# Optimization experiments

Measured on AMD Instinct MI355X. Metric: run time of the kernel, lower is better.

## Reference

```python
import jax, jax.numpy as jnp
import numpy as np
from jax import lax

R = 512          # num RoIs
K = 81           # num classes (COCO + bg)
IM_H, IM_W = 800, 1333
WX, WY, WW, WH = 10.0, 10.0, 5.0, 5.0   # cfg.MODEL.BBOX_REG_WEIGHTS
XFORM_CLIP = float(np.log(1000.0 / 16.0))  # cfg.BBOX_XFORM_CLIP
NMS_THRESH = 0.5
SCORE_THRESH = 0.001
MAX_PER_IMG = 100
POST_NMS_TOPN = 300


def setup_inputs() -> dict:
    key = jax.random.key(0)
    k1, k2, k3, k4, k5, k6 = jax.random.split(key, 6)
    # Build valid RoIs inside the image (x1<x2, y1<y2)
    cx = jax.random.uniform(k1, (R,)) * IM_W
    cy = jax.random.uniform(k2, (R,)) * IM_H
    w = jax.random.uniform(k3, (R,)) * 200.0 + 20.0
    h = jax.random.uniform(k4, (R,)) * 200.0 + 20.0
    rois = jnp.stack([
        jnp.clip(cx - 0.5 * w, 0.0, IM_W - 1),
        jnp.clip(cy - 0.5 * h, 0.0, IM_H - 1),
        jnp.clip(cx + 0.5 * w, 0.0, IM_W - 1),
        jnp.clip(cy + 0.5 * h, 0.0, IM_H - 1),
    ], axis=1).astype(jnp.float32)
    deltas = (jax.random.normal(k5, (R, 4 * K)) * 0.3).astype(jnp.float32)
    scores = jax.nn.softmax(jax.random.normal(k6, (R, K)) * 2.0, axis=1).astype(jnp.float32)
    return {"rois": rois, "deltas": deltas, "scores": scores}


def bbox_transform(boxes, deltas):
    # boxes [R,4], deltas [R,4K] -> pred boxes [R,K,4], clamped to image
    widths = boxes[:, 2] - boxes[:, 0] + 1.0
    heights = boxes[:, 3] - boxes[:, 1] + 1.0
    ctr_x = boxes[:, 0] + 0.5 * widths
    ctr_y = boxes[:, 1] + 0.5 * heights
    d = deltas.reshape(-1, K, 4)  # [R,K,4]
    dx = d[:, :, 0] / WX
    dy = d[:, :, 1] / WY
    dw = jnp.minimum(d[:, :, 2] / WW, XFORM_CLIP)
    dh = jnp.minimum(d[:, :, 3] / WH, XFORM_CLIP)
    pcx = dx * widths[:, None] + ctr_x[:, None]
    pcy = dy * heights[:, None] + ctr_y[:, None]
    pw = jnp.exp(dw) * widths[:, None]
    ph = jnp.exp(dh) * heights[:, None]
    x1 = jnp.clip(pcx - 0.5 * pw, 0.0, IM_W - 1)
    y1 = jnp.clip(pcy - 0.5 * ph, 0.0, IM_H - 1)
    x2 = jnp.clip(pcx + 0.5 * pw - 1.0, 0.0, IM_W - 1)
    y2 = jnp.clip(pcy + 0.5 * ph - 1.0, 0.0, IM_H - 1)
    return jnp.stack([x1, y1, x2, y2], axis=-1)  # [R,K,4]


def nms_one_class(scores_c, boxes_c):
    # Greedy NMS for one class. scores_c [R], boxes_c [R,4] -> keep mask [R] (orig order)
    order = jnp.argsort(-scores_c)
    b = boxes_c[order]
    areas = (b[:, 2] - b[:, 0] + 1.0) * (b[:, 3] - b[:, 1] + 1.0)
    xx1 = jnp.maximum(b[:, None, 0], b[None, :, 0])
    yy1 = jnp.maximum(b[:, None, 1], b[None, :, 1])
    xx2 = jnp.minimum(b[:, None, 2], b[None, :, 2])
    yy2 = jnp.minimum(b[:, None, 3], b[None, :, 3])
    inter = jnp.maximum(xx2 - xx1 + 1.0, 0.0) * jnp.maximum(yy2 - yy1 + 1.0, 0.0)
    iou = inter / (areas[:, None] + areas[None, :] - inter)
    suppress = iou > NMS_THRESH  # [R,R]
    idx = jnp.arange(R)

    def body(i, keep):
        sup = suppress[i] & keep[i] & (idx > i)
        return keep & (~sup)

    keep = lax.fori_loop(0, R, body, jnp.ones((R,), bool))
    keep = keep & (jnp.cumsum(keep) <= POST_NMS_TOPN)
    return jnp.zeros((R,), bool).at[order].set(keep)


def _detect(rois, deltas, scores):
    boxes3 = bbox_transform(rois, deltas)  # [R,K,4]
    # valid classes: max score over rois (excluding bg) above threshold
    cls_valid = jnp.concatenate([
        jnp.zeros((1,), bool),
        scores[:, 1:].max(axis=0) > SCORE_THRESH,
    ])  # [K]
    keep_kc = jax.vmap(nms_one_class, in_axes=(1, 1))(scores, boxes3)  # [K,R]
    nms_mask = (keep_kc.T & cls_valid[None, :]).astype(scores.dtype)  # [R,K]
    dists_all = nms_mask * scores
    # duplicate filtering: one label per box
    scores_pre = dists_all.max(axis=1)   # [R]
    labels_pre = dists_all.argmax(axis=1)
    order = jnp.argsort(-scores_pre)
    top = order[:MAX_PER_IMG]            # [100]
    scores_all = scores_pre[top]
    labels_all = labels_pre[top]
    valid = scores_all > SCORE_THRESH
    boxes_assign = boxes3.reshape(-1, 4)[top * K + labels_all]  # [100,4]
    scores_all = jnp.where(valid, scores_all, 0.0)
    boxes_assign = jnp.where(valid[:, None], boxes_assign, 0.0)
    out = jnp.concatenate([scores_all[:, None], boxes_assign], axis=1)  # [100,5]
    return out, labels_all, top


def reference(rois, deltas, scores):
    return _detect(rois, deltas, scores)
```

## Files before the change

### kernel.cpp

```cpp
#include <hip/hip_runtime.h>
#include <cstdint>
#include <cstddef>


#define R 512
#define K 81
#define IM_W_MAX 1332.0f
#define IM_H_MAX 799.0f
#define XFORM_CLIP_F 4.135166556742356f
#define NMS_THRESH_F 0.5f
#define SCORE_THRESH_F 0.001f
#define MAX_PER_IMG 100
#define POST_NMS_TOPN 300

__device__ __forceinline__ float4 transform_box(const float* __restrict__ rois,
                                                const float* __restrict__ deltas,
                                                int r, int k) {
    float4 roi = ((const float4*)rois)[r];
    float4 d4  = *(const float4*)(deltas + (size_t)r * (4 * K) + 4 * k);
    float w  = roi.z - roi.x + 1.0f;
    float h  = roi.w - roi.y + 1.0f;
    float cx = roi.x + 0.5f * w;
    float cy = roi.y + 0.5f * h;
    float dx = d4.x / 10.0f;
    float dy = d4.y / 10.0f;
    float dw = fminf(d4.z / 5.0f, XFORM_CLIP_F);
    float dh = fminf(d4.w / 5.0f, XFORM_CLIP_F);
    float pcx = dx * w + cx;
    float pcy = dy * h + cy;
    float pw  = expf(dw) * w;
    float ph  = expf(dh) * h;
    float4 b;
    b.x = fminf(fmaxf(pcx - 0.5f * pw, 0.0f), IM_W_MAX);
    b.y = fminf(fmaxf(pcy - 0.5f * ph, 0.0f), IM_H_MAX);
    b.z = fminf(fmaxf(pcx + 0.5f * pw - 1.0f, 0.0f), IM_W_MAX);
    b.w = fminf(fmaxf(pcy + 0.5f * ph - 1.0f, 0.0f), IM_H_MAX);
    return b;
}

__global__ void __launch_bounds__(512)
rank_boxes_kernel(const float* __restrict__ rois,
                  const float* __restrict__ deltas,
                  const float* __restrict__ scores,
                  float4* __restrict__ sbox_g,
                  int* __restrict__ order_g,
                  float* __restrict__ ssc_g,
                  int* __restrict__ valid_g) {
    const int k = blockIdx.x, tid = threadIdx.x;
    __shared__ unsigned long long s_key[R];
    __shared__ float s_red[R];

    const float sc = scores[tid * K + k];
    {
        unsigned int bits = __float_as_uint(sc);
        s_key[tid] = ((unsigned long long)(~bits) << 32) | (unsigned int)tid;
    }
    s_red[tid] = sc;
    __syncthreads();
    for (int s = 256; s > 0; s >>= 1) {
        if (tid < s) s_red[tid] = fmaxf(s_red[tid], s_red[tid + s]);
        __syncthreads();
    }
    const bool valid = (k != 0) && (s_red[0] > SCORE_THRESH_F);
    if (tid == 0) valid_g[k] = valid;
    if (!valid) return;

    const unsigned long long ki = s_key[tid];
    int cnt = 0;
    const ulonglong2* kp = (const ulonglong2*)s_key;
    #pragma unroll 8
    for (int j2 = 0; j2 < R / 2; ++j2) {
        ulonglong2 k2 = kp[j2];
        cnt += (k2.x < ki);
        cnt += (k2.y < ki);
    }
    sbox_g[k * R + cnt]  = transform_box(rois, deltas, tid, k);
    order_g[k * R + cnt] = tid;
    ssc_g[k * R + cnt]   = sc;
}

__device__ __forceinline__ bool iou_sup(float4 bi, float ai, float4 bj, float aj) {
    float xx1 = fmaxf(bi.x, bj.x);
    float yy1 = fmaxf(bi.y, bj.y);
    float xx2 = fminf(bi.z, bj.z);
    float yy2 = fminf(bi.w, bj.w);
    float iw = fmaxf(xx2 - xx1 + 1.0f, 0.0f);
    float ih = fmaxf(yy2 - yy1 + 1.0f, 0.0f);
    float inter = iw * ih;
    float denom = ai + aj - inter;
    float two_i = inter + inter;
    bool sup = two_i > denom * 1.0000002f;
    if (!sup && !(two_i < denom * 0.99999976f)) {
        sup = (inter / denom) > NMS_THRESH_F;
    }
    return sup;
}

__global__ void __launch_bounds__(256)
bitmatrix_kernel(const float4* __restrict__ sbox_g,
                 const int* __restrict__ valid_g,
                 unsigned long long* __restrict__ supT_g) {
    const int b = blockIdx.x;
    const int k = b >> 3;
    const int w = b & 7;
    const int tid = threadIdx.x;
    if (!valid_g[k]) return;

    __shared__ float4 s_jbox[64];
    __shared__ float  s_jarea[64];

    const int jbase = w * 64;
    if (tid < 64) {
        float4 bx = sbox_g[k * R + jbase + tid];
        s_jbox[tid]  = bx;
        s_jarea[tid] = (bx.z - bx.x + 1.0f) * (bx.w - bx.y + 1.0f);
    }

    const int i0 = tid;
    const float4 bi0 = sbox_g[k * R + i0];
    const float  ai0 = (bi0.z - bi0.x + 1.0f) * (bi0.w - bi0.y + 1.0f);

    const unsigned long long* dummy;
    (void)dummy;

    if (w < 4) {
        __syncthreads();
        const int d0 = i0 - jbase;
        unsigned long long mask0 =
            (d0 < 0) ? ~0ull : ((d0 >= 63) ? 0ull : (~0ull << (d0 + 1)));
        unsigned long long bits0 = 0ull;
        if (mask0) {
            #pragma unroll 8
            for (int jj = 0; jj < 64; ++jj) {
                float4 bj = s_jbox[jj];
                float  aj = s_jarea[jj];
                bits0 |= (unsigned long long)iou_sup(bi0, ai0, bj, aj) << jj;
            }
        }
        supT_g[k * 4096 + w * 512 + i0]       = bits0 & mask0;
        supT_g[k * 4096 + w * 512 + i0 + 256] = 0ull;
    } else {
        const int i1 = i0 + 256;
        const float4 bi1 = sbox_g[k * R + i1];
        const float  ai1 = (bi1.z - bi1.x + 1.0f) * (bi1.w - bi1.y + 1.0f);
        __syncthreads();
        const int d1 = i1 - jbase;
        unsigned long long mask1 =
            (d1 < 0) ? ~0ull : ((d1 >= 63) ? 0ull : (~0ull << (d1 + 1)));
        unsigned long long bits0 = 0ull, bits1 = 0ull;
        if (__ballot(mask1 != 0ull)) {
            #pragma unroll 8
            for (int jj = 0; jj < 64; ++jj) {
                float4 bj = s_jbox[jj];
                float  aj = s_jarea[jj];
                bits0 |= (unsigned long long)iou_sup(bi0, ai0, bj, aj) << jj;
                bits1 |= (unsigned long long)iou_sup(bi1, ai1, bj, aj) << jj;
            }
        } else {
            #pragma unroll 8
            for (int jj = 0; jj < 64; ++jj) {
                float4 bj = s_jbox[jj];
                float  aj = s_jarea[jj];
                bits0 |= (unsigned long long)iou_sup(bi0, ai0, bj, aj) << jj;
            }
        }
        supT_g[k * 4096 + w * 512 + i0] = bits0;
        supT_g[k * 4096 + w * 512 + i1] = bits1 & mask1;
    }
}

__global__ void __launch_bounds__(64)
sweep_kernel(const unsigned long long* __restrict__ supT_g,
             const int* __restrict__ order_g,
             const float* __restrict__ ssc_g,
             const int* __restrict__ valid_g,
             float* __restrict__ dists_t) {
    const int k = blockIdx.x;
    const int l = threadIdx.x;

    if (!valid_g[k]) {
        #pragma unroll
        for (int p = 0; p < 8; ++p) dists_t[k * R + p * 64 + l] = 0.0f;
        return;
    }

    int   ord[8];
    float ssc[8];
    #pragma unroll
    for (int p = 0; p < 8; ++p) {
        ord[p] = order_g[k * R + p * 64 + l];
        ssc[p] = ssc_g[k * R + p * 64 + l];
    }

    const unsigned long long* base = supT_g + (size_t)k * 4096;
    unsigned long long rrow[8], rnext[8];
    #pragma unroll
    for (int w = 0; w < 8; ++w) rrow[w] = base[w * 512 + l];

    unsigned long long kb[8];
    #pragma unroll
    for (int w = 0; w < 8; ++w) kb[w] = ~0ull;

    #pragma unroll
    for (int wb = 0; wb < 8; ++wb) {
        if (wb < 7) {
            #pragma unroll
            for (int w = 0; w < 8; ++w)
                rnext[w] = (w > wb) ? base[w * 512 + (wb + 1) * 64 + l] : 0ull;
        }

        const unsigned long long nz = __ballot(rrow[wb] != 0ull);
        unsigned long long cur = kb[wb];
        unsigned long long m = cur & nz;
        while (m) {
            int bit = __builtin_ctzll(m);
            const unsigned int r_lo = (unsigned int)(rrow[wb] & 0xffffffffull);
            const unsigned int r_hi = (unsigned int)(rrow[wb] >> 32);
            unsigned long long row =
                ((unsigned long long)(unsigned int)__builtin_amdgcn_readlane((int)r_hi, bit) << 32) |
                 (unsigned long long)(unsigned int)__builtin_amdgcn_readlane((int)r_lo, bit);
            m &= m - 1;
            cur &= ~row;
            m   &= ~row;
        }
        kb[wb] = cur;

        #pragma unroll
        for (int w = wb + 1; w < 8; ++w) {
            unsigned long long contrib = ((cur >> l) & 1ull) ? rrow[w] : 0ull;
            if (__ballot(contrib != 0ull)) {
                #pragma unroll
                for (int off = 32; off > 0; off >>= 1)
                    contrib |= __shfl_xor(contrib, off, 64);
                kb[w] &= ~contrib;
            }
        }

        #pragma unroll
        for (int w = 0; w < 8; ++w) rrow[w] = rnext[w];
    }

    int total = 0;
    #pragma unroll
    for (int w = 0; w < 8; ++w) total += __popcll(kb[w]);
    if (total > POST_NMS_TOPN) {
        int cnt = 0;
        #pragma unroll
        for (int w = 0; w < 8; ++w) {
            int pc = __popcll(kb[w]);
            if (cnt + pc <= POST_NMS_TOPN) { cnt += pc; continue; }
            unsigned long long word = kb[w], outw = 0ull;
            int room = POST_NMS_TOPN - cnt;
            while (room > 0) {
                unsigned long long lsb = word & (~word + 1ull);
                outw |= lsb; word ^= lsb; --room;
            }
            kb[w] = outw; cnt = POST_NMS_TOPN;
        }
    }

    #pragma unroll
    for (int p = 0; p < 8; ++p)
        dists_t[k * R + ord[p]] = ((kb[p] >> l) & 1ull) ? ssc[p] : 0.0f;
}

__global__ void __launch_bounds__(512)
finalize_kernel(const float* __restrict__ dists_t,
                const float* __restrict__ rois,
                const float* __restrict__ deltas,
                float* __restrict__ out) {
    const int b = blockIdx.x;
    const int t = threadIdx.x;
    __shared__ unsigned long long s_key[R];
    __shared__ int s_arg[R];

    {
        const int r = t;
        float vmax = dists_t[r];
        int arg = 0;
        #pragma unroll 8
        for (int kk = 1; kk < K; ++kk) {
            float v = dists_t[kk * R + r];
            if (v > vmax) { vmax = v; arg = kk; }
        }
        unsigned int bits = __float_as_uint(vmax);
        s_key[r] = ((unsigned long long)(~bits) << 32) | (unsigned int)r;
        s_arg[r] = arg;
    }
    __syncthreads();

    const int ri = b * 64 + (t >> 3);
    const int c  = t & 7;
    const unsigned long long ki = s_key[ri];
    int cnt = 0;
    #pragma unroll 8
    for (int j = 0; j < 64; ++j) {
        int jj = (j + c * 8) & 63;
        cnt += (s_key[c * 64 + jj] < ki);
    }
    cnt += __shfl_xor(cnt, 1, 64);
    cnt += __shfl_xor(cnt, 2, 64);
    cnt += __shfl_xor(cnt, 4, 64);

    if (c == 0 && cnt < MAX_PER_IMG) {
        float vmax = __uint_as_float(~(unsigned int)(ki >> 32));
        int arg = s_arg[ri];
        bool valid = vmax > SCORE_THRESH_F;
        float4 bx = transform_box(rois, deltas, ri, arg);
        out[cnt * 5 + 0] = valid ? vmax : 0.0f;
        out[cnt * 5 + 1] = valid ? bx.x : 0.0f;
        out[cnt * 5 + 2] = valid ? bx.y : 0.0f;
        out[cnt * 5 + 3] = valid ? bx.z : 0.0f;
        out[cnt * 5 + 4] = valid ? bx.w : 0.0f;
        out[500 + cnt] = (float)arg;
        out[600 + cnt] = (float)ri;
    }
}

extern "C" void kernel_launch(void* const* d_in, const int* in_sizes, int n_in,
                              void* d_out, int out_size, void* d_ws, size_t ws_size,
                              hipStream_t stream) {
    const float* rois   = (const float*)d_in[0];
    const float* deltas = (const float*)d_in[1];
    const float* scores = (const float*)d_in[2];
    float* out = (float*)d_out;

    char* ws = (char*)d_ws;
    float4* sbox_g  = (float4*)(ws + 0);
    int*    order_g = (int*)   (ws + 663552);
    float*  ssc_g   = (float*) (ws + 829440);
    int*    valid_g = (int*)   (ws + 995328);
    float*  dists_t = (float*) (ws + 995840);
    unsigned long long* supT_g = (unsigned long long*)(ws + 1161728);

    rank_boxes_kernel<<<K, 512, 0, stream>>>(rois, deltas, scores,
                                             sbox_g, order_g, ssc_g, valid_g);
    bitmatrix_kernel <<<K * 8, 256, 0, stream>>>(sbox_g, valid_g, supT_g);
    sweep_kernel     <<<K, 64, 0, stream>>>(supT_g, order_g, ssc_g, valid_g, dists_t);
    finalize_kernel  <<<8, 512, 0, stream>>>(dists_t, rois, deltas, out);
}
```

Measured before the change: 106.0 us.

## Fuse NMS bitmatrix and sweep kernels with a last-block-done counter

Merges the suppression bitmatrix kernel and the greedy sweep kernel into one launch. Each class's 8 blocks bump a per-class atomic counter, and the last block to finish runs the sweep for that class, reading the bitmatrix with agent-scope atomic loads. This removes one kernel launch and its inter-kernel gap, and lets sweeps for early classes overlap with bitmatrix work for other classes. It also drops the redundant zero stores for the unused lower-triangle words. The cost is a per-class counter reset in the rank kernel. There is some memory-ordering risk, because the stores are relaxed and no explicit fence comes before the counter increment.

```diff
diff --git a/kernel.cpp b/kernel.cpp
--- a/kernel.cpp
+++ b/kernel.cpp
@@ -12,6 +12,15 @@
 #define SCORE_THRESH_F 0.001f
 #define MAX_PER_IMG 100
 #define POST_NMS_TOPN 300
+
+__device__ __forceinline__ void store_agent_u64(unsigned long long* p,
+                                                unsigned long long v) {
+    __hip_atomic_store(p, v, __ATOMIC_RELAXED, __HIP_MEMORY_SCOPE_AGENT);
+}
+__device__ __forceinline__ unsigned long long load_agent_u64(
+        const unsigned long long* p) {
+    return __hip_atomic_load(p, __ATOMIC_RELAXED, __HIP_MEMORY_SCOPE_AGENT);
+}
 
 __device__ __forceinline__ float4 transform_box(const float* __restrict__ rois,
                                                 const float* __restrict__ deltas,
@@ -38,47 +47,6 @@
     return b;
 }
 
-__global__ void __launch_bounds__(512)
-rank_boxes_kernel(const float* __restrict__ rois,
-                  const float* __restrict__ deltas,
-                  const float* __restrict__ scores,
-                  float4* __restrict__ sbox_g,
-                  int* __restrict__ order_g,
-                  float* __restrict__ ssc_g,
-                  int* __restrict__ valid_g) {
-    const int k = blockIdx.x, tid = threadIdx.x;
-    __shared__ unsigned long long s_key[R];
-    __shared__ float s_red[R];
-
-    const float sc = scores[tid * K + k];
-    {
-        unsigned int bits = __float_as_uint(sc);
-        s_key[tid] = ((unsigned long long)(~bits) << 32) | (unsigned int)tid;
-    }
-    s_red[tid] = sc;
-    __syncthreads();
-    for (int s = 256; s > 0; s >>= 1) {
-        if (tid < s) s_red[tid] = fmaxf(s_red[tid], s_red[tid + s]);
-        __syncthreads();
-    }
-    const bool valid = (k != 0) && (s_red[0] > SCORE_THRESH_F);
-    if (tid == 0) valid_g[k] = valid;
-    if (!valid) return;
-
-    const unsigned long long ki = s_key[tid];
-    int cnt = 0;
-    const ulonglong2* kp = (const ulonglong2*)s_key;
-    #pragma unroll 8
-    for (int j2 = 0; j2 < R / 2; ++j2) {
-        ulonglong2 k2 = kp[j2];
-        cnt += (k2.x < ki);
-        cnt += (k2.y < ki);
-    }
-    sbox_g[k * R + cnt]  = transform_box(rois, deltas, tid, k);
-    order_g[k * R + cnt] = tid;
-    ssc_g[k * R + cnt]   = sc;
-}
-
 __device__ __forceinline__ bool iou_sup(float4 bi, float ai, float4 bj, float aj) {
     float xx1 = fmaxf(bi.x, bj.x);
     float yy1 = fmaxf(bi.y, bj.y);
@@ -96,89 +64,134 @@
     return sup;
 }
 
+__global__ void __launch_bounds__(512)
+rank_boxes_kernel(const float* __restrict__ rois,
+                  const float* __restrict__ deltas,
+                  const float* __restrict__ scores,
+                  float4* __restrict__ sbox_g,
+                  int* __restrict__ order_g,
+                  float* __restrict__ ssc_g,
+                  int* __restrict__ valid_g,
+                  int* __restrict__ done_k) {
+    const int k = blockIdx.x, tid = threadIdx.x;
+    __shared__ unsigned long long s_key[R];
+    __shared__ float s_red[R];
+
+    const float sc = scores[tid * K + k];
+    {
+        unsigned int bits = __float_as_uint(sc);
+        s_key[tid] = ((unsigned long long)(~bits) << 32) | (unsigned int)tid;
+    }
+    s_red[tid] = sc;
+    __syncthreads();
+    for (int s = 256; s > 0; s >>= 1) {
+        if (tid < s) s_red[tid] = fmaxf(s_red[tid], s_red[tid + s]);
+        __syncthreads();
+    }
+    const bool valid = (k != 0) && (s_red[0] > SCORE_THRESH_F);
+    if (tid == 0) { valid_g[k] = valid; done_k[k] = 0; }
+    if (!valid) return;
+
+    const unsigned long long ki = s_key[tid];
+    int cnt = 0;
+    const ulonglong2* kp = (const ulonglong2*)s_key;
+    #pragma unroll 8
+    for (int j2 = 0; j2 < R / 2; ++j2) {
+        ulonglong2 k2 = kp[j2];
+        cnt += (k2.x < ki);
+        cnt += (k2.y < ki);
+    }
+    sbox_g[k * R + cnt]  = transform_box(rois, deltas, tid, k);
+    order_g[k * R + cnt] = tid;
+    ssc_g[k * R + cnt]   = sc;
+}
+
 __global__ void __launch_bounds__(256)
-bitmatrix_kernel(const float4* __restrict__ sbox_g,
-                 const int* __restrict__ valid_g,
-                 unsigned long long* __restrict__ supT_g) {
+bitmega_kernel(const float4* __restrict__ sbox_g,
+               const int* __restrict__ valid_g,
+               unsigned long long* __restrict__ supT_g,
+               const int* __restrict__ order_g,
+               const float* __restrict__ ssc_g,
+               int* __restrict__ done_k,
+               float* __restrict__ dists_t) {
     const int b = blockIdx.x;
     const int k = b >> 3;
     const int w = b & 7;
     const int tid = threadIdx.x;
-    if (!valid_g[k]) return;
 
     __shared__ float4 s_jbox[64];
     __shared__ float  s_jarea[64];
-
+    __shared__ int    s_closer;
+
+    const bool valid = valid_g[k] != 0;
     const int jbase = w * 64;
-    if (tid < 64) {
-        float4 bx = sbox_g[k * R + jbase + tid];
-        s_jbox[tid]  = bx;
-        s_jarea[tid] = (bx.z - bx.x + 1.0f) * (bx.w - bx.y + 1.0f);
-    }
-
-    const int i0 = tid;
-    const float4 bi0 = sbox_g[k * R + i0];
-    const float  ai0 = (bi0.z - bi0.x + 1.0f) * (bi0.w - bi0.y + 1.0f);
-
-    const unsigned long long* dummy;
-    (void)dummy;
-
-    if (w < 4) {
+
+    if (valid) {
+        if (tid < 64) {
+            float4 bx = sbox_g[k * R + jbase + tid];
+            s_jbox[tid]  = bx;
+            s_jarea[tid] = (bx.z - bx.x + 1.0f) * (bx.w - bx.y + 1.0f);
+        }
+        const int i0 = tid;
+        const float4 bi0 = sbox_g[k * R + i0];
+        const float  ai0 = (bi0.z - bi0.x + 1.0f) * (bi0.w - bi0.y + 1.0f);
+
+        if (w < 4) {
+            __syncthreads();
+            const int d0 = i0 - jbase;
+            unsigned long long mask0 =
+                (d0 < 0) ? ~0ull : ((d0 >= 63) ? 0ull : (~0ull << (d0 + 1)));
+            unsigned long long bits0 = 0ull;
+            if (mask0) {
+                #pragma unroll 8
+                for (int jj = 0; jj < 64; ++jj) {
+                    float4 bj = s_jbox[jj];
+                    float  aj = s_jarea[jj];
+                    bits0 |= (unsigned long long)iou_sup(bi0, ai0, bj, aj) << jj;
+                }
+            }
+            store_agent_u64(&supT_g[k * 4096 + w * 512 + i0], bits0 & mask0);
+        } else {
+            const int i1 = i0 + 256;
+            const float4 bi1 = sbox_g[k * R + i1];
+            const float  ai1 = (bi1.z - bi1.x + 1.0f) * (bi1.w - bi1.y + 1.0f);
+            __syncthreads();
+            const int d1 = i1 - jbase;
+            unsigned long long mask1 =
+                (d1 < 0) ? ~0ull : ((d1 >= 63) ? 0ull : (~0ull << (d1 + 1)));
+            unsigned long long bits0 = 0ull, bits1 = 0ull;
+            if (__ballot(mask1 != 0ull)) {
+                #pragma unroll 8
+                for (int jj = 0; jj < 64; ++jj) {
+                    float4 bj = s_jbox[jj];
+                    float  aj = s_jarea[jj];
+                    bits0 |= (unsigned long long)iou_sup(bi0, ai0, bj, aj) << jj;
+                    bits1 |= (unsigned long long)iou_sup(bi1, ai1, bj, aj) << jj;
+                }
+            } else {
+                #pragma unroll 8
+                for (int jj = 0; jj < 64; ++jj) {
+                    float4 bj = s_jbox[jj];
+                    float  aj = s_jarea[jj];
+                    bits0 |= (unsigned long long)iou_sup(bi0, ai0, bj, aj) << jj;
+                }
+            }
+            store_agent_u64(&supT_g[k * 4096 + w * 512 + i0], bits0);
+            store_agent_u64(&supT_g[k * 4096 + w * 512 + i1], bits1 & mask1);
+        }
+    } else {
         __syncthreads();
-        const int d0 = i0 - jbase;
-        unsigned long long mask0 =
-            (d0 < 0) ? ~0ull : ((d0 >= 63) ? 0ull : (~0ull << (d0 + 1)));
-        unsigned long long bits0 = 0ull;
-        if (mask0) {
-            #pragma unroll 8
-            for (int jj = 0; jj < 64; ++jj) {
-                float4 bj = s_jbox[jj];
-                float  aj = s_jarea[jj];
-                bits0 |= (unsigned long long)iou_sup(bi0, ai0, bj, aj) << jj;
-            }
-        }
-        supT_g[k * 4096 + w * 512 + i0]       = bits0 & mask0;
-        supT_g[k * 4096 + w * 512 + i0 + 256] = 0ull;
-    } else {
-        const int i1 = i0 + 256;
-        const float4 bi1 = sbox_g[k * R + i1];
-        const float  ai1 = (bi1.z - bi1.x + 1.0f) * (bi1.w - bi1.y + 1.0f);
-        __syncthreads();
-        const int d1 = i1 - jbase;
-        unsigned long long mask1 =
-            (d1 < 0) ? ~0ull : ((d1 >= 63) ? 0ull : (~0ull << (d1 + 1)));
-        unsigned long long bits0 = 0ull, bits1 = 0ull;
-        if (__ballot(mask1 != 0ull)) {
-            #pragma unroll 8
-            for (int jj = 0; jj < 64; ++jj) {
-                float4 bj = s_jbox[jj];
-                float  aj = s_jarea[jj];
-                bits0 |= (unsigned long long)iou_sup(bi0, ai0, bj, aj) << jj;
-                bits1 |= (unsigned long long)iou_sup(bi1, ai1, bj, aj) << jj;
-            }
-        } else {
-            #pragma unroll 8
-            for (int jj = 0; jj < 64; ++jj) {
-                float4 bj = s_jbox[jj];
-                float  aj = s_jarea[jj];
-                bits0 |= (unsigned long long)iou_sup(bi0, ai0, bj, aj) << jj;
-            }
-        }
-        supT_g[k * 4096 + w * 512 + i0] = bits0;
-        supT_g[k * 4096 + w * 512 + i1] = bits1 & mask1;
-    }
-}
-
-__global__ void __launch_bounds__(64)
-sweep_kernel(const unsigned long long* __restrict__ supT_g,
-             const int* __restrict__ order_g,
-             const float* __restrict__ ssc_g,
-             const int* __restrict__ valid_g,
-             float* __restrict__ dists_t) {
-    const int k = blockIdx.x;
-    const int l = threadIdx.x;
-
-    if (!valid_g[k]) {
+    }
+
+    __syncthreads();
+    if (tid == 0) s_closer = (atomicAdd(&done_k[k], 1) == 7);
+    __syncthreads();
+    if (!s_closer) return;
+
+    if (tid >= 64) return;
+    const int l = tid;
+
+    if (!valid) {
         #pragma unroll
         for (int p = 0; p < 8; ++p) dists_t[k * R + p * 64 + l] = 0.0f;
         return;
@@ -192,21 +205,23 @@
         ssc[p] = ssc_g[k * R + p * 64 + l];
     }
 
-    const unsigned long long* base = supT_g + (size_t)k * 4096;
+    unsigned long long* base = supT_g + (size_t)k * 4096;
     unsigned long long rrow[8], rnext[8];
     #pragma unroll
-    for (int w = 0; w < 8; ++w) rrow[w] = base[w * 512 + l];
+    for (int w2 = 0; w2 < 8; ++w2)
+        rrow[w2] = load_agent_u64(&base[w2 * 512 + l]);
 
     unsigned long long kb[8];
     #pragma unroll
-    for (int w = 0; w < 8; ++w) kb[w] = ~0ull;
+    for (int w2 = 0; w2 < 8; ++w2) kb[w2] = ~0ull;
 
     #pragma unroll
     for (int wb = 0; wb < 8; ++wb) {
         if (wb < 7) {
             #pragma unroll
-            for (int w = 0; w < 8; ++w)
-                rnext[w] = (w > wb) ? base[w * 512 + (wb + 1) * 64 + l] : 0ull;
+            for (int w2 = 0; w2 < 8; ++w2)
+                rnext[w2] = (w2 > wb)
+                    ? load_agent_u64(&base[w2 * 512 + (wb + 1) * 64 + l]) : 0ull;
         }
 
         const unsigned long long nz = __ballot(rrow[wb] != 0ull);
@@ -226,36 +241,36 @@
         kb[wb] = cur;
 
         #pragma unroll
-        for (int w = wb + 1; w < 8; ++w) {
-            unsigned long long contrib = ((cur >> l) & 1ull) ? rrow[w] : 0ull;
+        for (int w2 = wb + 1; w2 < 8; ++w2) {
+            unsigned long long contrib = ((cur >> l) & 1ull) ? rrow[w2] : 0ull;
             if (__ballot(contrib != 0ull)) {
                 #pragma unroll
                 for (int off = 32; off > 0; off >>= 1)
                     contrib |= __shfl_xor(contrib, off, 64);
-                kb[w] &= ~contrib;
+                kb[w2] &= ~contrib;
             }
         }
 
         #pragma unroll
-        for (int w = 0; w < 8; ++w) rrow[w] = rnext[w];
+        for (int w2 = 0; w2 < 8; ++w2) rrow[w2] = rnext[w2];
     }
 
     int total = 0;
     #pragma unroll
-    for (int w = 0; w < 8; ++w) total += __popcll(kb[w]);
+    for (int w2 = 0; w2 < 8; ++w2) total += __popcll(kb[w2]);
     if (total > POST_NMS_TOPN) {
         int cnt = 0;
         #pragma unroll
-        for (int w = 0; w < 8; ++w) {
-            int pc = __popcll(kb[w]);
+        for (int w2 = 0; w2 < 8; ++w2) {
+            int pc = __popcll(kb[w2]);
             if (cnt + pc <= POST_NMS_TOPN) { cnt += pc; continue; }
-            unsigned long long word = kb[w], outw = 0ull;
+            unsigned long long word = kb[w2], outw = 0ull;
             int room = POST_NMS_TOPN - cnt;
             while (room > 0) {
                 unsigned long long lsb = word & (~word + 1ull);
                 outw |= lsb; word ^= lsb; --room;
             }
-            kb[w] = outw; cnt = POST_NMS_TOPN;
+            kb[w2] = outw; cnt = POST_NMS_TOPN;
         }
     }
 
@@ -332,10 +347,12 @@
     int*    valid_g = (int*)   (ws + 995328);
     float*  dists_t = (float*) (ws + 995840);
     unsigned long long* supT_g = (unsigned long long*)(ws + 1161728);
+    int*    done_k  = (int*)   (ws + 3815936);
 
     rank_boxes_kernel<<<K, 512, 0, stream>>>(rois, deltas, scores,
-                                             sbox_g, order_g, ssc_g, valid_g);
-    bitmatrix_kernel <<<K * 8, 256, 0, stream>>>(sbox_g, valid_g, supT_g);
-    sweep_kernel     <<<K, 64, 0, stream>>>(supT_g, order_g, ssc_g, valid_g, dists_t);
+                                             sbox_g, order_g, ssc_g,
+                                             valid_g, done_k);
+    bitmega_kernel   <<<K * 8, 256, 0, stream>>>(sbox_g, valid_g, supT_g,
+                                                 order_g, ssc_g, done_k, dists_t);
     finalize_kernel  <<<8, 512, 0, stream>>>(dists_t, rois, deltas, out);
 }
```

Measured after the change: 106.4 us. About the same (+0.4%).
